# Kernel tuning notes

Hardware: AMD Instinct MI355X
Metric: run time of the kernel (lower is better)

The kernel has to match this reference:

```python
import jax, jax.numpy as jnp
import numpy as np

D = 128; H = 4; DK = D // H; ZN = 64; V = 8

def _silu(x):
    return x * jax.nn.sigmoid(x)

def _mlp3(x, w1, b1, w2, b2, w3, b3):
    h = _silu(x @ w1 + b1)
    h = _silu(h @ w2 + b2)
    return h @ w3 + b3

def _snorm(x):
    # StaticLayerNorm: center, divide by unbiased std (torch .std default ddof=1)
    c = x - jnp.mean(x, axis=-1, keepdims=True)
    std = jnp.sqrt(jnp.sum(c * c, axis=-1, keepdims=True) / (x.shape[-1] - 1))
    std = jnp.where(std == 0, 1.0, std)
    return c / std

def setup_inputs():
    key = jax.random.key(0)
    ks = list(jax.random.split(key, 40)); ki = iter(ks)
    xs = (6.0 / (DK + D)) ** 0.5
    inp = {}
    inp["latent"] = jax.random.normal(next(ki), (ZN, D, V, V, V), jnp.float32)
    inp["nodes"] = jax.random.normal(next(ki), (ZN, D), jnp.float32)
    inp["t"] = jax.random.uniform(next(ki), (ZN,), jnp.float32)
    for nm in ("qw", "kw", "vw"):
        inp[nm] = jax.random.uniform(next(ki), (H, D, DK), jnp.float32, -xs, xs)
    for nm in ("qb", "kb", "vb"):
        inp[nm] = jnp.zeros((H, DK), jnp.float32)
    inp["ow"] = jax.random.normal(next(ki), (D, D), jnp.float32) * (1.0 / D) ** 0.5
    for pre, dout in (("an_gb", 2 * D), ("an_a", D), ("fn_gb", 2 * D), ("fn_a", D)):
        inp[pre + "_w1"] = jax.random.normal(next(ki), (D, D), jnp.float32) * 0.05
        inp[pre + "_b1"] = jnp.zeros((D,), jnp.float32)
        inp[pre + "_w2"] = jax.random.normal(next(ki), (D, D), jnp.float32) * 0.05
        inp[pre + "_b2"] = jnp.zeros((D,), jnp.float32)
        inp[pre + "_w3"] = jax.random.normal(next(ki), (D, dout), jnp.float32) * 0.05
        inp[pre + "_b3"] = jnp.zeros((dout,), jnp.float32)
    return inp

def reference(latent, nodes, t, qw, kw, vw, qb, kb, vb, ow,
              an_gb_w1, an_gb_b1, an_gb_w2, an_gb_b2, an_gb_w3, an_gb_b3,
              an_a_w1, an_a_b1, an_a_w2, an_a_b2, an_a_w3, an_a_b3,
              fn_gb_w1, fn_gb_b1, fn_gb_w2, fn_gb_b2, fn_gb_w3, fn_gb_b3,
              fn_a_w1, fn_a_b1, fn_a_w2, fn_a_b2, fn_a_w3, fn_a_b3):
    b, d, vx, vy, vz = latent.shape
    n = vx * vy * vz
    x = latent.reshape(b, d, n).transpose(0, 2, 1)  # [b, n, d]
    cond = nodes[:, None, :] + t[:, None, None]     # [b, 1, d]
    gb1 = _mlp3(cond, an_gb_w1, an_gb_b1, an_gb_w2, an_gb_b2, an_gb_w3, an_gb_b3)
    g1, be1 = jnp.split(gb1, 2, axis=-1)
    al1 = _mlp3(cond, an_a_w1, an_a_b1, an_a_w2, an_a_b2, an_a_w3, an_a_b3)
    gb2 = _mlp3(cond, fn_gb_w1, fn_gb_b1, fn_gb_w2, fn_gb_b2, fn_gb_w3, fn_gb_b3)
    g2, be2 = jnp.split(gb2, 2, axis=-1)
    al2 = _mlp3(cond, fn_a_w1, fn_a_b1, fn_a_w2, fn_a_b2, fn_a_w3, fn_a_b3)
    # FAITHFUL BUG REPRO: source unpacks adaLN's (gamma, beta, alpha) as (alpha, gamma, beta)
    alpha1, gamma1, beta1 = g1, be1, al1
    alpha2, gamma2, beta2 = g2, be2, al2
    x2 = gamma1 * _snorm(x) + beta1
    dk = d // qw.shape[0]
    Q = jnp.einsum('bnd,hdk->bhnk', x2, qw) + qb[None, :, None, :]
    K = jnp.einsum('bnd,hdk->bhnk', x2, kw) + kb[None, :, None, :]
    Vv = jnp.einsum('bnd,hdk->bhnk', x2, vw) + vb[None, :, None, :]
    S = jnp.einsum('bhnk,bhmk->bhnm', Q, K) / (dk ** 0.5)
    P = jax.nn.softmax(S, axis=-1)
    O = jnp.einsum('bhnm,bhmk->bhnk', P, Vv)
    O = O.transpose(0, 2, 3, 1).reshape(b, n, d)  # matches torch permute(0,2,3,1).reshape
    attn = O @ ow
    x = x + alpha1 * attn
    x2 = gamma2 * _snorm(x) + beta2
    x = x + alpha2 * x2  # NOTE: source forward never applies self.ffn (dead module)
    return x.transpose(0, 2, 1).reshape(b, d, vx, vy, vz)
```

## Files before the change

### kernel.cpp

```cpp
#include <hip/hip_runtime.h>
#include <hip/hip_bf16.h>
#include <math.h>


#define NB 64

typedef __attribute__((ext_vector_type(8))) short bf16x8;
typedef __attribute__((ext_vector_type(4))) float f32x4;

__device__ __forceinline__ float silu_f(float x) { return x / (1.0f + __expf(-x)); }
__device__ __forceinline__ unsigned short f2bf(float x) {
    __hip_bfloat16 h = __float2bfloat16(x);
    return *reinterpret_cast<unsigned short*>(&h);
}

__global__ void __launch_bounds__(128) k_cond(
    const float* __restrict__ nodes, const float* __restrict__ tv,
    const float* __restrict__ w10, const float* __restrict__ b10,
    const float* __restrict__ w20, const float* __restrict__ b20,
    const float* __restrict__ w30, const float* __restrict__ b30,
    const float* __restrict__ w11, const float* __restrict__ b11,
    const float* __restrict__ w21, const float* __restrict__ b21,
    const float* __restrict__ w31, const float* __restrict__ b31,
    const float* __restrict__ w12, const float* __restrict__ b12,
    const float* __restrict__ w22, const float* __restrict__ b22,
    const float* __restrict__ w32, const float* __restrict__ b32,
    const float* __restrict__ w13, const float* __restrict__ b13,
    const float* __restrict__ w23, const float* __restrict__ b23,
    const float* __restrict__ w33, const float* __restrict__ b33,
    float* __restrict__ mods)
{
    int blk = blockIdx.x;
    int b = blk >> 2, m = blk & 3;
    const float* W1 = m==0?w10 : m==1?w11 : m==2?w12 : w13;
    const float* B1 = m==0?b10 : m==1?b11 : m==2?b12 : b13;
    const float* W2 = m==0?w20 : m==1?w21 : m==2?w22 : w23;
    const float* B2 = m==0?b20 : m==1?b21 : m==2?b22 : b23;
    const float* W3 = m==0?w30 : m==1?w31 : m==2?w32 : w33;
    const float* B3 = m==0?b30 : m==1?b31 : m==2?b32 : b33;
    int dout256 = (m == 0 || m == 2);
    int slot = (m==0)?0 : (m==1)?2 : (m==2)?3 : 5;

    __shared__ float xs[128], h1[128], h2[128];
    int t = threadIdx.x;
    xs[t] = nodes[b*128 + t] + tv[b];
    __syncthreads();

    float acc = B1[t];
    for (int i = 0; i < 128; i++) acc += xs[i] * W1[i*128 + t];
    h1[t] = silu_f(acc);
    __syncthreads();

    acc = B2[t];
    for (int i = 0; i < 128; i++) acc += h1[i] * W2[i*128 + t];
    h2[t] = silu_f(acc);
    __syncthreads();

    if (dout256) {
        float a0 = B3[t], a1 = B3[t + 128];
        for (int i = 0; i < 128; i++) {
            float h = h2[i];
            a0 += h * W3[i*256 + t];
            a1 += h * W3[i*256 + t + 128];
        }
        mods[((size_t)b*6 + slot    )*128 + t] = a0;
        mods[((size_t)b*6 + slot + 1)*128 + t] = a1;
    } else {
        float a0 = B3[t];
        for (int i = 0; i < 128; i++) a0 += h2[i] * W3[i*128 + t];
        mods[((size_t)b*6 + slot)*128 + t] = a0;
    }
}

__global__ void __launch_bounds__(256, 1) k_norm_qkv(
    const float* __restrict__ latent, const float* __restrict__ mods,
    const float* __restrict__ qw, const float* __restrict__ kw, const float* __restrict__ vw,
    const float* __restrict__ qb, const float* __restrict__ kb, const float* __restrict__ vb,
    unsigned short* __restrict__ Qb, unsigned short* __restrict__ Kb,
    unsigned short* __restrict__ Vtb)
{
    __shared__ float xs[64*129];
    __shared__ unsigned short xb[64*136];
    __shared__ unsigned short WtS[128*136];
    __shared__ float g1s[128], be1s[128], mean_s[64], rstd_s[64];

    int blk = blockIdx.x;
    int b = blk >> 3, n0 = (blk & 7) * 64;
    int t = threadIdx.x;

    if (t < 128) {
        g1s[t]  = mods[((size_t)b*6 + 1)*128 + t];
        be1s[t] = mods[((size_t)b*6 + 2)*128 + t];
    }
    const float* lp = latent + (size_t)b*65536 + n0;
    for (int idx = t; idx < 8192; idx += 256) {
        int d = idx >> 6, j = idx & 63;
        xs[j*129 + d] = lp[(size_t)d*512 + j];
    }
    __syncthreads();

    {
        int row = t >> 2, sub = t & 3;
        float s = 0.f, ss = 0.f;
        const float* xr = &xs[row*129 + sub*32];
        #pragma unroll
        for (int i = 0; i < 32; i++) { float v = xr[i]; s += v; ss += v*v; }
        s += __shfl_xor(s, 1); ss += __shfl_xor(ss, 1);
        s += __shfl_xor(s, 2); ss += __shfl_xor(ss, 2);
        float mean = s * (1.0f/128.0f);
        float var = (ss - 128.0f*mean*mean) * (1.0f/127.0f);
        var = var < 0.f ? 0.f : var;
        float sd = sqrtf(var);
        mean_s[row] = mean;
        rstd_s[row] = (sd == 0.f) ? 1.f : 1.f/sd;
    }
    __syncthreads();

    for (int idx = t; idx < 8192; idx += 256) {
        int j = idx >> 7, d = idx & 127;
        float v = xs[j*129 + d];
        xb[j*136 + d] = f2bf(g1s[d]*((v - mean_s[j]) * rstd_s[j]) + be1s[d]);
    }
    __syncthreads();

    int w = t >> 6, lane = t & 63, lo = lane & 15, hi = lane >> 4;

    bf16x8 af[4];
    #pragma unroll
    for (int kc = 0; kc < 4; kc++)
        af[kc] = *(const bf16x8*)(xb + (w*16 + lo)*136 + kc*32 + hi*8);

    const f32x4 zero = {0.f, 0.f, 0.f, 0.f};
    const float qscale = 0.17677669529663687f;

    #pragma unroll 1
    for (int ph = 0; ph < 3; ph++) {
        const float* wp = ph==0 ? qw : (ph==1 ? kw : vw);
        __syncthreads();
        for (int idx = t; idx < 16384; idx += 256) {
            int kk = idx & 31, d = (idx >> 5) & 127, h = idx >> 12;
            WtS[(h*32 + kk)*136 + d] = f2bf(wp[idx]);
        }
        __syncthreads();

        for (int nt = 0; nt < 8; nt++) {
            f32x4 acc = zero;
            #pragma unroll
            for (int kc = 0; kc < 4; kc++) {
                bf16x8 bf = *(const bf16x8*)(WtS + (nt*16 + lo)*136 + kc*32 + hi*8);
                acc = __builtin_amdgcn_mfma_f32_16x16x32_bf16(af[kc], bf, acc, 0, 0, 0);
            }
            int c = nt*16 + lo, h = c >> 5, kk = c & 31;
            size_t bh = (size_t)(b*4 + h);
            if (ph == 0) {
                float bias = qb[c];
                #pragma unroll
                for (int j = 0; j < 4; j++) {
                    int n = n0 + w*16 + hi*4 + j;
                    Qb[(bh*512 + n)*32 + kk] = f2bf((acc[j] + bias) * qscale);
                }
            } else if (ph == 1) {
                float bias = kb[c];
                #pragma unroll
                for (int j = 0; j < 4; j++) {
                    int n = n0 + w*16 + hi*4 + j;
                    Kb[(bh*512 + n)*32 + kk] = f2bf(acc[j] + bias);
                }
            } else {
                float bias = vb[c];
                #pragma unroll
                for (int j = 0; j < 4; j++) {
                    int nl = w*16 + hi*4 + j;
                    xb[c*68 + nl] = f2bf(acc[j] + bias);
                }
            }
        }
    }
    __syncthreads();
    for (int idx = t; idx < 8192; idx += 256) {
        int c = idx >> 6, j = idx & 63;
        int h = c >> 5, kk = c & 31;
        size_t bh = (size_t)(b*4 + h);
        Vtb[(bh*32 + kk)*512 + n0 + j] = xb[c*68 + j];
    }
}

__global__ void __launch_bounds__(256, 1) k_attn(
    const unsigned short* __restrict__ Qb, const unsigned short* __restrict__ Kb,
    const unsigned short* __restrict__ Vtb, unsigned short* __restrict__ Ob)
{
    __shared__ unsigned short KsS[512*32];
    __shared__ unsigned short VsS[32*512];
    __shared__ unsigned short Ps[4][16*512];

    int bh = blockIdx.x;
    int t = threadIdx.x;

    const unsigned short* kgp = Kb + (size_t)bh*512*32;
    const unsigned short* vgp = Vtb + (size_t)bh*32*512;
    for (int idx = t; idx < 2048; idx += 256) {
        *(bf16x8*)(KsS + idx*8) = *(const bf16x8*)(kgp + idx*8);
    }
    for (int idx = t; idx < 2048; idx += 256) {
        int r = idx >> 6, cch = idx & 63;
        *(bf16x8*)(VsS + r*512 + ((cch*8) ^ ((r&7)<<3))) =
            *(const bf16x8*)(vgp + r*512 + cch*8);
    }
    __syncthreads();

    int w = t >> 6, lane = t & 63, lo = lane & 15, hi = lane >> 4;
    unsigned short* Pw = &Ps[w][0];
    const unsigned short* qbase = Qb + (size_t)bh*512*32;

    const f32x4 zero = {0.f, 0.f, 0.f, 0.f};
    int b = bh >> 2, h = bh & 3;

    for (int qt = 0; qt < 8; ++qt) {
        int q0 = w*128 + qt*16;
        bf16x8 qa = *(const bf16x8*)(qbase + (size_t)(q0 + lo)*32 + hi*8);

        f32x4 s[32];
        #pragma unroll
        for (int kt = 0; kt < 32; ++kt) {
            bf16x8 kf = *(const bf16x8*)(KsS + (kt*16 + lo)*32 + hi*8);
            s[kt] = __builtin_amdgcn_mfma_f32_16x16x32_bf16(qa, kf, zero, 0, 0, 0);
        }

        float mrow[4] = {-1e30f, -1e30f, -1e30f, -1e30f};
        #pragma unroll
        for (int kt = 0; kt < 32; ++kt) {
            #pragma unroll
            for (int j = 0; j < 4; ++j) mrow[j] = fmaxf(mrow[j], s[kt][j]);
        }
        #pragma unroll
        for (int j = 0; j < 4; ++j) {
            #pragma unroll
            for (int off = 1; off < 16; off <<= 1)
                mrow[j] = fmaxf(mrow[j], __shfl_xor(mrow[j], off));
        }

        float ssum[4] = {0.f, 0.f, 0.f, 0.f};
        #pragma unroll
        for (int kt = 0; kt < 32; ++kt) {
            #pragma unroll
            for (int j = 0; j < 4; ++j) {
                float p = __expf(s[kt][j] - mrow[j]);
                ssum[j] += p;
                int row = hi*4 + j;
                Pw[row*512 + ((kt*16 + lo) ^ ((row&7)<<3))] = f2bf(p);
            }
        }
        #pragma unroll
        for (int j = 0; j < 4; ++j) {
            #pragma unroll
            for (int off = 1; off < 16; off <<= 1)
                ssum[j] += __shfl_xor(ssum[j], off);
        }

        f32x4 oa = zero, ob = zero;
        const unsigned short* Pl = Pw + lo*512;
        const unsigned short* Vl0 = VsS + lo*512;
        const unsigned short* Vl1 = VsS + (16 + lo)*512;
        int swz = (lo & 7) << 3;
        #pragma unroll
        for (int cc = 0; cc < 16; ++cc) {
            int off = (cc*32 + hi*8) ^ swz;
            bf16x8 pa = *(const bf16x8*)(Pl + off);
            bf16x8 v0 = *(const bf16x8*)(Vl0 + off);
            bf16x8 v1 = *(const bf16x8*)(Vl1 + off);
            oa = __builtin_amdgcn_mfma_f32_16x16x32_bf16(pa, v0, oa, 0, 0, 0);
            ob = __builtin_amdgcn_mfma_f32_16x16x32_bf16(pa, v1, ob, 0, 0, 0);
        }

        unsigned short* op = Ob + ((size_t)(b*512 + q0 + hi*4))*128 + h;
        #pragma unroll
        for (int j = 0; j < 4; ++j) {
            float invj = 1.f / ssum[j];
            op[(size_t)j*128 + lo*4]        = f2bf(oa[j] * invj);
            op[(size_t)j*128 + (lo+16)*4]   = f2bf(ob[j] * invj);
        }
    }
}

__global__ void __launch_bounds__(256, 2) k_out(
    const float* __restrict__ latent, const unsigned short* __restrict__ Ob,
    const float* __restrict__ ow, const float* __restrict__ mods,
    float* __restrict__ outp)
{
    __shared__ unsigned short owT[128*136];
    __shared__ float xs[64*129];
    __shared__ float a1s[128], a2s[128], g2s[128], b2s[128];
    __shared__ float mean_s[64], rstd_s[64];

    int blk = blockIdx.x;
    int b = blk >> 3, n0 = (blk & 7) * 64;
    int t = threadIdx.x;

    if (t < 128) {
        a1s[t] = mods[((size_t)b*6 + 0)*128 + t];
        a2s[t] = mods[((size_t)b*6 + 3)*128 + t];
        g2s[t] = mods[((size_t)b*6 + 4)*128 + t];
        b2s[t] = mods[((size_t)b*6 + 5)*128 + t];
    }
    for (int idx = t; idx < 16384; idx += 256) {
        int i = idx >> 7, c = idx & 127;
        owT[c*136 + i] = f2bf(ow[idx]);
    }
    const float* lp = latent + (size_t)b*65536 + n0;
    for (int idx = t; idx < 8192; idx += 256) {
        int d = idx >> 6, j = idx & 63;
        xs[j*129 + d] = lp[(size_t)d*512 + j];
    }
    __syncthreads();

    int w = t >> 6, lane = t & 63, lo = lane & 15, hi = lane >> 4;

    const unsigned short* arow = Ob + ((size_t)(b*512 + n0 + w*16 + lo))*128;
    bf16x8 af[4];
    #pragma unroll
    for (int kc = 0; kc < 4; kc++)
        af[kc] = *(const bf16x8*)(arow + kc*32 + hi*8);

    const f32x4 zero = {0.f, 0.f, 0.f, 0.f};
    for (int nt = 0; nt < 8; nt++) {
        f32x4 acc = zero;
        #pragma unroll
        for (int kc = 0; kc < 4; kc++) {
            bf16x8 bf = *(const bf16x8*)(owT + (nt*16 + lo)*136 + kc*32 + hi*8);
            acc = __builtin_amdgcn_mfma_f32_16x16x32_bf16(af[kc], bf, acc, 0, 0, 0);
        }
        int c = nt*16 + lo;
        #pragma unroll
        for (int j = 0; j < 4; j++) {
            int nl = w*16 + hi*4 + j;
            xs[nl*129 + c] += a1s[c] * acc[j];
        }
    }
    __syncthreads();

    {
        int row = t >> 2, sub = t & 3;
        float s = 0.f, ss = 0.f;
        const float* xr = &xs[row*129 + sub*32];
        #pragma unroll
        for (int i = 0; i < 32; i++) { float v = xr[i]; s += v; ss += v*v; }
        s += __shfl_xor(s, 1); ss += __shfl_xor(ss, 1);
        s += __shfl_xor(s, 2); ss += __shfl_xor(ss, 2);
        float mean = s * (1.0f/128.0f);
        float var = (ss - 128.0f*mean*mean) * (1.0f/127.0f);
        var = var < 0.f ? 0.f : var;
        float sd = sqrtf(var);
        mean_s[row] = mean;
        rstd_s[row] = (sd == 0.f) ? 1.f : 1.f/sd;
    }
    __syncthreads();

    float* outb = outp + (size_t)b*65536 + n0;
    for (int idx = t; idx < 8192; idx += 256) {
        int d = idx >> 6, j = idx & 63;
        float v = xs[j*129 + d];
        float nv = (v - mean_s[j]) * rstd_s[j];
        outb[(size_t)d*512 + j] = v + a2s[d]*(g2s[d]*nv + b2s[d]);
    }
}

extern "C" void kernel_launch(void* const* d_in, const int* in_sizes, int n_in,
                              void* d_out, int out_size, void* d_ws, size_t ws_size,
                              hipStream_t stream) {
    const float* latent = (const float*)d_in[0];
    const float* nodes  = (const float*)d_in[1];
    const float* tv     = (const float*)d_in[2];
    const float* qw     = (const float*)d_in[3];
    const float* kw     = (const float*)d_in[4];
    const float* vw     = (const float*)d_in[5];
    const float* qb     = (const float*)d_in[6];
    const float* kb     = (const float*)d_in[7];
    const float* vb     = (const float*)d_in[8];
    const float* owp    = (const float*)d_in[9];

    const float* mw[24];
    for (int i = 0; i < 24; i++) mw[i] = (const float*)d_in[10 + i];

    char* wsb = (char*)d_ws;
    unsigned short* Qb  = (unsigned short*)(wsb);
    unsigned short* Kb  = (unsigned short*)(wsb + 8388608);
    unsigned short* Vtb = (unsigned short*)(wsb + 16777216);
    unsigned short* Ob  = (unsigned short*)(wsb + 25165824);
    float* mods = (float*)(wsb + 33554432);

    float* outp = (float*)d_out;

    k_cond<<<dim3(NB*4), dim3(128), 0, stream>>>(
        nodes, tv,
        mw[0], mw[1], mw[2], mw[3], mw[4], mw[5],
        mw[6], mw[7], mw[8], mw[9], mw[10], mw[11],
        mw[12], mw[13], mw[14], mw[15], mw[16], mw[17],
        mw[18], mw[19], mw[20], mw[21], mw[22], mw[23],
        mods);

    k_norm_qkv<<<dim3(NB*8), dim3(256), 0, stream>>>(
        latent, mods, qw, kw, vw, qb, kb, vb, Qb, Kb, Vtb);

    k_attn<<<dim3(NB*4), dim3(256), 0, stream>>>(Qb, Kb, Vtb, Ob);

    k_out<<<dim3(NB*8), dim3(256), 0, stream>>>(latent, Ob, owp, mods, outp);
}
```

Measured before the change: 246.5 us.

## Keep softmax probabilities in registers via transposed MFMA and doubled waves

The attention kernel computes S transposed (K as A operand) so each lane owns one query row. This reduces max and sum reductions to two shuffles, and the probabilities are moved into the PV MFMA operand layout with cross-lane shuffles instead of a shared-memory P buffer. The log2(e) factor is folded into the Q scale so raw exp2 can be used. Blocks grow to 512 threads with 2 blocks per CU, and the freed LDS allows more concurrent waves. The cost is many extra shuffles per PV step and higher register pressure from the 64 packed probability registers under the tighter launch bound.

```diff
diff --git a/kernel.cpp b/kernel.cpp
--- a/kernel.cpp
+++ b/kernel.cpp
@@ -131,7 +131,7 @@
         af[kc] = *(const bf16x8*)(xb + (w*16 + lo)*136 + kc*32 + hi*8);
 
     const f32x4 zero = {0.f, 0.f, 0.f, 0.f};
-    const float qscale = 0.17677669529663687f;
+    const float qscale = 0.17677669529663687f * 1.4426950408889634f;
 
     #pragma unroll 1
     for (int ph = 0; ph < 3; ph++) {
@@ -185,23 +185,21 @@
     }
 }
 
-__global__ void __launch_bounds__(256, 1) k_attn(
+__global__ void __launch_bounds__(512, 2) k_attn(
     const unsigned short* __restrict__ Qb, const unsigned short* __restrict__ Kb,
     const unsigned short* __restrict__ Vtb, unsigned short* __restrict__ Ob)
 {
     __shared__ unsigned short KsS[512*32];
     __shared__ unsigned short VsS[32*512];
-    __shared__ unsigned short Ps[4][16*512];
 
     int bh = blockIdx.x;
     int t = threadIdx.x;
 
     const unsigned short* kgp = Kb + (size_t)bh*512*32;
     const unsigned short* vgp = Vtb + (size_t)bh*32*512;
-    for (int idx = t; idx < 2048; idx += 256) {
+    for (int idx = t; idx < 2048; idx += 512)
         *(bf16x8*)(KsS + idx*8) = *(const bf16x8*)(kgp + idx*8);
-    }
-    for (int idx = t; idx < 2048; idx += 256) {
+    for (int idx = t; idx < 2048; idx += 512) {
         int r = idx >> 6, cch = idx & 63;
         *(bf16x8*)(VsS + r*512 + ((cch*8) ^ ((r&7)<<3))) =
             *(const bf16x8*)(vgp + r*512 + cch*8);
@@ -209,75 +207,79 @@
     __syncthreads();
 
     int w = t >> 6, lane = t & 63, lo = lane & 15, hi = lane >> 4;
-    unsigned short* Pw = &Ps[w][0];
     const unsigned short* qbase = Qb + (size_t)bh*512*32;
-
     const f32x4 zero = {0.f, 0.f, 0.f, 0.f};
     int b = bh >> 2, h = bh & 3;
 
-    for (int qt = 0; qt < 8; ++qt) {
-        int q0 = w*128 + qt*16;
+    const unsigned short* Vl0 = VsS + lo*512;
+    const unsigned short* Vl1 = VsS + (16 + lo)*512;
+    int swz = (lo & 7) << 3;
+    int srcA = lo + 32*(hi & 1);
+
+    for (int qt = 0; qt < 4; ++qt) {
+        int q0 = w*64 + qt*16;
         bf16x8 qa = *(const bf16x8*)(qbase + (size_t)(q0 + lo)*32 + hi*8);
 
         f32x4 s[32];
         #pragma unroll
         for (int kt = 0; kt < 32; ++kt) {
             bf16x8 kf = *(const bf16x8*)(KsS + (kt*16 + lo)*32 + hi*8);
-            s[kt] = __builtin_amdgcn_mfma_f32_16x16x32_bf16(qa, kf, zero, 0, 0, 0);
-        }
-
-        float mrow[4] = {-1e30f, -1e30f, -1e30f, -1e30f};
+            s[kt] = __builtin_amdgcn_mfma_f32_16x16x32_bf16(kf, qa, zero, 0, 0, 0);
+        }
+
+        float m = -1e30f;
+        #pragma unroll
+        for (int kt = 0; kt < 32; ++kt)
+            m = fmaxf(m, fmaxf(fmaxf(s[kt][0], s[kt][1]), fmaxf(s[kt][2], s[kt][3])));
+        m = fmaxf(m, __shfl_xor(m, 16));
+        m = fmaxf(m, __shfl_xor(m, 32));
+
+        float sum = 0.f;
+        unsigned int pw0[32], pw1[32];
         #pragma unroll
         for (int kt = 0; kt < 32; ++kt) {
-            #pragma unroll
-            for (int j = 0; j < 4; ++j) mrow[j] = fmaxf(mrow[j], s[kt][j]);
-        }
-        #pragma unroll
-        for (int j = 0; j < 4; ++j) {
-            #pragma unroll
-            for (int off = 1; off < 16; off <<= 1)
-                mrow[j] = fmaxf(mrow[j], __shfl_xor(mrow[j], off));
-        }
-
-        float ssum[4] = {0.f, 0.f, 0.f, 0.f};
-        #pragma unroll
-        for (int kt = 0; kt < 32; ++kt) {
-            #pragma unroll
-            for (int j = 0; j < 4; ++j) {
-                float p = __expf(s[kt][j] - mrow[j]);
-                ssum[j] += p;
-                int row = hi*4 + j;
-                Pw[row*512 + ((kt*16 + lo) ^ ((row&7)<<3))] = f2bf(p);
-            }
-        }
-        #pragma unroll
-        for (int j = 0; j < 4; ++j) {
-            #pragma unroll
-            for (int off = 1; off < 16; off <<= 1)
-                ssum[j] += __shfl_xor(ssum[j], off);
-        }
+            float p0 = __builtin_amdgcn_exp2f(s[kt][0] - m);
+            float p1 = __builtin_amdgcn_exp2f(s[kt][1] - m);
+            float p2 = __builtin_amdgcn_exp2f(s[kt][2] - m);
+            float p3 = __builtin_amdgcn_exp2f(s[kt][3] - m);
+            sum += (p0 + p1) + (p2 + p3);
+            pw0[kt] = (unsigned)f2bf(p0) | ((unsigned)f2bf(p1) << 16);
+            pw1[kt] = (unsigned)f2bf(p2) | ((unsigned)f2bf(p3) << 16);
+        }
+        sum += __shfl_xor(sum, 16);
+        sum += __shfl_xor(sum, 32);
 
         f32x4 oa = zero, ob = zero;
-        const unsigned short* Pl = Pw + lo*512;
-        const unsigned short* Vl0 = VsS + lo*512;
-        const unsigned short* Vl1 = VsS + (16 + lo)*512;
-        int swz = (lo & 7) << 3;
-        #pragma unroll
-        for (int cc = 0; cc < 16; ++cc) {
-            int off = (cc*32 + hi*8) ^ swz;
-            bf16x8 pa = *(const bf16x8*)(Pl + off);
+        #pragma unroll
+        for (int kt2 = 0; kt2 < 16; ++kt2) {
+            unsigned e0 = pw0[2*kt2],     e1 = pw1[2*kt2];
+            unsigned o0 = pw0[2*kt2 + 1], o1 = pw1[2*kt2 + 1];
+            unsigned ae0 = (unsigned)__shfl((int)e0, srcA, 64);
+            unsigned ae1 = (unsigned)__shfl((int)e1, srcA, 64);
+            unsigned ao0 = (unsigned)__shfl((int)o0, srcA, 64);
+            unsigned ao1 = (unsigned)__shfl((int)o1, srcA, 64);
+            unsigned be0 = (unsigned)__shfl((int)e0, srcA + 16, 64);
+            unsigned be1 = (unsigned)__shfl((int)e1, srcA + 16, 64);
+            unsigned bo0 = (unsigned)__shfl((int)o0, srcA + 16, 64);
+            unsigned bo1 = (unsigned)__shfl((int)o1, srcA + 16, 64);
+            union { unsigned u[4]; bf16x8 v; } pb;
+            pb.u[0] = (hi < 2) ? ae0 : ao0;
+            pb.u[1] = (hi < 2) ? ae1 : ao1;
+            pb.u[2] = (hi < 2) ? be0 : bo0;
+            pb.u[3] = (hi < 2) ? be1 : bo1;
+            int off = (kt2*32 + hi*8) ^ swz;
             bf16x8 v0 = *(const bf16x8*)(Vl0 + off);
             bf16x8 v1 = *(const bf16x8*)(Vl1 + off);
-            oa = __builtin_amdgcn_mfma_f32_16x16x32_bf16(pa, v0, oa, 0, 0, 0);
-            ob = __builtin_amdgcn_mfma_f32_16x16x32_bf16(pa, v1, ob, 0, 0, 0);
-        }
-
-        unsigned short* op = Ob + ((size_t)(b*512 + q0 + hi*4))*128 + h;
+            oa = __builtin_amdgcn_mfma_f32_16x16x32_bf16(v0, pb.v, oa, 0, 0, 0);
+            ob = __builtin_amdgcn_mfma_f32_16x16x32_bf16(v1, pb.v, ob, 0, 0, 0);
+        }
+
+        float inv = 1.f / sum;
+        unsigned short* op = Ob + ((size_t)(b*512 + q0 + lo))*128 + h;
         #pragma unroll
         for (int j = 0; j < 4; ++j) {
-            float invj = 1.f / ssum[j];
-            op[(size_t)j*128 + lo*4]        = f2bf(oa[j] * invj);
-            op[(size_t)j*128 + (lo+16)*4]   = f2bf(ob[j] * invj);
+            op[(hi*4 + j)*4]       = f2bf(oa[j] * inv);
+            op[(16 + hi*4 + j)*4]  = f2bf(ob[j] * inv);
         }
     }
 }
@@ -401,7 +403,7 @@
     k_norm_qkv<<<dim3(NB*8), dim3(256), 0, stream>>>(
         latent, mods, qw, kw, vw, qb, kb, vb, Qb, Kb, Vtb);
 
-    k_attn<<<dim3(NB*4), dim3(256), 0, stream>>>(Qb, Kb, Vtb, Ob);
+    k_attn<<<dim3(NB*4), dim3(512), 0, stream>>>(Qb, Kb, Vtb, Ob);
 
     k_out<<<dim3(NB*8), dim3(256), 0, stream>>>(latent, Ob, owp, mods, outp);
 }
```

New measurement: 278.6 us. 13.0% more time.
